# Kernel optimization log

Hardware: AMD Instinct MI355X
Metric: run time of the kernel (lower is better)

Reference implementation:

```python
import jax, jax.numpy as jnp
import numpy as np

# Module hyperparameters (match init_kwargs)
N_HEADS = 8
N_EMB = 64          # == window_size; unfolded window becomes the embed dim
WINDOW_SIZE = 64
STRIDE = 32
HEAD_DIM = N_EMB // N_HEADS


def _unfold_last(x):
    """torch.Tensor.unfold on last dim: [..., L] -> [..., NW, WINDOW_SIZE]."""
    L = x.shape[-1]
    starts = jnp.arange(0, L - WINDOW_SIZE + 1, STRIDE)          # [NW]
    idx = starts[:, None] + jnp.arange(WINDOW_SIZE)[None, :]     # [NW, WS]
    return x[..., idx]


def setup_inputs() -> dict:
    key = jax.random.key(0)
    ks = jax.random.split(key, 7)
    S, L = 512, 2048
    q = jax.random.normal(ks[0], (S, L), jnp.float32)
    k = jax.random.normal(ks[1], (S, L), jnp.float32)
    v = jax.random.normal(ks[2], (S, L), jnp.float32)
    scale = 1.0 / np.sqrt(N_EMB)
    in_proj_weight = jax.random.normal(ks[3], (3 * N_EMB, N_EMB), jnp.float32) * scale
    in_proj_bias = jax.random.normal(ks[4], (3 * N_EMB,), jnp.float32) * 0.02
    out_proj_weight = jax.random.normal(ks[5], (N_EMB, N_EMB), jnp.float32) * scale
    out_proj_bias = jax.random.normal(ks[6], (N_EMB,), jnp.float32) * 0.02
    return {"q": q, "k": k, "v": v,
            "in_proj_weight": in_proj_weight, "in_proj_bias": in_proj_bias,
            "out_proj_weight": out_proj_weight, "out_proj_bias": out_proj_bias}


def reference(q, k, v, in_proj_weight, in_proj_bias, out_proj_weight, out_proj_bias):
    # Unfold last dim into overlapping windows: [S, L] -> [S, NW, E]
    qu, ku, vu = _unfold_last(q), _unfold_last(k), _unfold_last(v)
    S, NW, E = qu.shape

    # nn.MultiheadAttention input projections (packed in_proj)
    Wq, Wk, Wv = jnp.split(in_proj_weight, 3, axis=0)
    bq, bk, bv = jnp.split(in_proj_bias, 3, axis=0)
    qp = qu @ Wq.T + bq   # [S, NW, E]
    kp = ku @ Wk.T + bk
    vp = vu @ Wv.T + bv

    # Split heads: [S, NW, E] -> [NW, H, S, HD]  (MHA: seq=S, batch=NW)
    def heads(x):
        return x.reshape(S, NW, N_HEADS, HEAD_DIM).transpose(1, 2, 0, 3)
    qh, kh, vh = heads(qp), heads(kp), heads(vp)

    scale = 1.0 / np.sqrt(HEAD_DIM)
    scores = jnp.einsum("nhsd,nhtd->nhst", qh, kh) * scale   # [NW, H, S, S]
    attn = jax.nn.softmax(scores, axis=-1)
    ctx = jnp.einsum("nhst,nhtd->nhsd", attn, vh)            # [NW, H, S, HD]

    # Merge heads back to [S, NW, E], then output projection
    ctx = ctx.transpose(2, 0, 1, 3).reshape(S, NW, E)
    x = ctx @ out_proj_weight.T + out_proj_bias              # [S, NW, E]

    # average_attn_weights=True (torch default): mean over heads -> [NW, S, S]
    attn_weights = attn.mean(axis=1)
    return x, attn_weights
```

## Files before the change

kernel.cpp:

```cpp
#include <hip/hip_runtime.h>

#define S_DIM 512
#define L_DIM 2048
#define NW 63
#define E_DIM 64

typedef __bf16 bf16_t;
typedef __bf16 bf16x8 __attribute__((ext_vector_type(8)));
typedef float f32x4 __attribute__((ext_vector_type(4)));
typedef _Float16 f16_t;
typedef _Float16 f16x2 __attribute__((ext_vector_type(2)));
typedef _Float16 f16x4 __attribute__((ext_vector_type(4)));

__device__ inline bf16x8 cvt8(const float* __restrict__ p) {
    float4 a = *(const float4*)p;
    float4 b = *(const float4*)(p + 4);
    bf16x8 r;
    r[0] = (bf16_t)a.x; r[1] = (bf16_t)a.y; r[2] = (bf16_t)a.z; r[3] = (bf16_t)a.w;
    r[4] = (bf16_t)b.x; r[5] = (bf16_t)b.y; r[6] = (bf16_t)b.z; r[7] = (bf16_t)b.w;
    return r;
}

__device__ inline f16x2 pkrtz(float a, float b) {
    return __builtin_bit_cast(f16x2, __builtin_amdgcn_cvt_pkrtz(a, b));
}

__global__ __launch_bounds__(512) void swa_proj(
    const float* __restrict__ q, const float* __restrict__ k,
    const float* __restrict__ v, const float* __restrict__ w,
    const float* __restrict__ bias,
    f16_t* __restrict__ qpg, f16_t* __restrict__ kpg, f16_t* __restrict__ vpg)
{
    __shared__ __align__(16) f16_t stq[128][72];
    __shared__ __align__(16) f16_t stk[128][72];
    __shared__ __align__(16) f16_t vt[64][136];

    int tid = threadIdx.x, lane = tid & 63, wave = tid >> 6;
    int bid = blockIdx.x;
    int n = bid >> 2, rg = bid & 3;
    int ml = lane & 15, quad = lane >> 4;
    int srow = wave * 16;
    int s0 = rg * 128 + srow;
    int arow = (s0 + ml) * L_DIM + 32 * n + quad * 8;
    const float cs = 0.35355339059327373f * 1.4426950408889634f;

    bf16x8 qa0 = cvt8(q + arow), qa1 = cvt8(q + arow + 32);
    bf16x8 ka0 = cvt8(k + arow), ka1 = cvt8(k + arow + 32);
    bf16x8 va0 = cvt8(v + arow), va1 = cvt8(v + arow + 32);

#pragma unroll
    for (int et = 0; et < 4; ++et) {
        bf16x8 wq0 = cvt8(w + (et * 16 + ml) * 64 + quad * 8);
        bf16x8 wq1 = cvt8(w + (et * 16 + ml) * 64 + 32 + quad * 8);
        bf16x8 wk0 = cvt8(w + (64 + et * 16 + ml) * 64 + quad * 8);
        bf16x8 wk1 = cvt8(w + (64 + et * 16 + ml) * 64 + 32 + quad * 8);
        bf16x8 wv0 = cvt8(w + (128 + et * 16 + ml) * 64 + quad * 8);
        bf16x8 wv1 = cvt8(w + (128 + et * 16 + ml) * 64 + 32 + quad * 8);

        float bq = bias[et * 16 + ml];
        float bk = bias[64 + et * 16 + ml];
        float bv = bias[128 + et * 16 + ml];
        f32x4 qacc = (f32x4){bq, bq, bq, bq};
        f32x4 kacc = (f32x4){bk, bk, bk, bk};
        f32x4 vacc = (f32x4){bv, bv, bv, bv};
        qacc = __builtin_amdgcn_mfma_f32_16x16x32_bf16(qa0, wq0, qacc, 0, 0, 0);
        qacc = __builtin_amdgcn_mfma_f32_16x16x32_bf16(qa1, wq1, qacc, 0, 0, 0);
        kacc = __builtin_amdgcn_mfma_f32_16x16x32_bf16(ka0, wk0, kacc, 0, 0, 0);
        kacc = __builtin_amdgcn_mfma_f32_16x16x32_bf16(ka1, wk1, kacc, 0, 0, 0);
        vacc = __builtin_amdgcn_mfma_f32_16x16x32_bf16(va0, wv0, vacc, 0, 0, 0);
        vacc = __builtin_amdgcn_mfma_f32_16x16x32_bf16(va1, wv1, vacc, 0, 0, 0);

#pragma unroll
        for (int rr = 0; rr < 4; ++rr) {
            int row = srow + quad * 4 + rr;
            stq[row][et * 16 + ml] = (f16_t)(qacc[rr] * cs);
            stk[row][et * 16 + ml] = (f16_t)kacc[rr];
            vt[et * 16 + ml][row]  = (f16_t)vacc[rr];
        }
    }
    __syncthreads();

    {
        const size_t qbase = ((size_t)n * S_DIM + rg * 128) * 64;
#pragma unroll
        for (int c = tid; c < 1024; c += 512) {
            int row = c >> 3, col = (c & 7) * 8;
            *(uint4*)(qpg + qbase + (size_t)row * 64 + col) = *(const uint4*)&stq[row][col];
        }
    }
    {
#pragma unroll
        for (int c = tid; c < 1024; c += 512) {
            int et = c >> 8, cc = c & 255, row = cc >> 1, hf = cc & 1;
            *(uint4*)(kpg + (((size_t)n * 4 + et) * S_DIM + rg * 128 + row) * 16 + hf * 8) =
                *(const uint4*)&stk[row][et * 16 + hf * 8];
        }
    }
    {
#pragma unroll
        for (int c = tid; c < 1024; c += 512) {
            int vr = c >> 4, sc = c & 15;
            *(uint4*)(vpg + (((size_t)n * 4 + (vr >> 4)) * 16 + (vr & 15)) * S_DIM +
                      rg * 128 + sc * 8) = *(const uint4*)&vt[vr][sc * 8];
        }
    }
}

__global__ __launch_bounds__(512, 2) void swa_attn(
    const f16_t* __restrict__ qpg, const f16_t* __restrict__ kpg,
    const f16_t* __restrict__ vpg, const float* __restrict__ wout,
    const float* __restrict__ bout, float* __restrict__ out)
{
    __shared__ __align__(16) f16_t kp_s[S_DIM][18];
    __shared__ __align__(16) f16_t vp_t[16][520];
    __shared__ __align__(16) f16_t qp_t[2][16][68];
    __shared__ __align__(16) f16_t zstub[8];
    __shared__ __align__(16) float wsum_s[2][2][16][4];
    __shared__ __align__(16) f16_t ctxslot[2][4][2][16][8];
    __shared__ float  ctx_s[32][68];
    __shared__ bf16_t wo_t[64][66];
    __shared__ float  bo_s[64];

    int tid = threadIdx.x, lane = tid & 63, wave = tid >> 6;
    int wg = wave >> 1, m = wave & 1;
    int bid = blockIdx.x;
    int n = bid >> 4, tile = bid & 15, srow0 = tile * 32;
    int ml = lane & 15, quad = lane >> 4;
    bool hi = lane >= 32;

    float* out_x  = out;
    float* out_aw = out + (size_t)S_DIM * NW * E_DIM;

#pragma unroll
    for (int i = 0; i < 8; ++i) {
        int idx = tid + i * 512;
        wo_t[idx & 63][idx >> 6] = (bf16_t)wout[idx];
    }
    if (tid < 64) bo_s[tid] = bout[tid];
    if (tid < 8)  zstub[tid] = (f16_t)0.f;
    {
        int row = tid >> 4, c = tid & 15;
        f16x4 qv = *(const f16x4*)(qpg + ((size_t)n * S_DIM + srow0 + row) * 64 + c * 4);
        *(f16x4*)&qp_t[row >> 4][row & 15][c * 4] = qv;
    }

    int idx0 = tid, idx1 = tid + 512;
    uint4 ldk0, ldk1, ldv0, ldv1;
    {
        const f16_t* kb = kpg + ((size_t)n * 4 + 0) * S_DIM * 16;
        ldk0 = *(const uint4*)(kb + (idx0 >> 1) * 16 + (idx0 & 1) * 8);
        ldk1 = *(const uint4*)(kb + (idx1 >> 1) * 16 + (idx1 & 1) * 8);
        const f16_t* vb = vpg + ((size_t)n * 4 + 0) * 16 * S_DIM;
        ldv0 = *(const uint4*)(vb + (idx0 >> 6) * S_DIM + (idx0 & 63) * 8);
        ldv1 = *(const uint4*)(vb + (idx1 >> 6) * S_DIM + (idx1 & 63) * 8);
    }

    f32x4 aacc[8];
#pragma unroll
    for (int t = 0; t < 8; ++t) aacc[t] = (f32x4){0.f, 0.f, 0.f, 0.f};

    for (int hp = 0; hp < 4; ++hp) {
        *(uint4*)&kp_s[idx0 >> 1][(idx0 & 1) * 8] = ldk0;
        *(uint4*)&kp_s[idx1 >> 1][(idx1 & 1) * 8] = ldk1;
        *(uint4*)&vp_t[idx0 >> 6][(idx0 & 63) * 8] = ldv0;
        *(uint4*)&vp_t[idx1 >> 6][(idx1 & 63) * 8] = ldv1;
        if (hp < 3) {
            const f16_t* kb = kpg + ((size_t)n * 4 + hp + 1) * S_DIM * 16;
            ldk0 = *(const uint4*)(kb + (idx0 >> 1) * 16 + (idx0 & 1) * 8);
            ldk1 = *(const uint4*)(kb + (idx1 >> 1) * 16 + (idx1 & 1) * 8);
            const f16_t* vb = vpg + ((size_t)n * 4 + hp + 1) * 16 * S_DIM;
            ldv0 = *(const uint4*)(vb + (idx0 >> 6) * S_DIM + (idx0 & 63) * 8);
            ldv1 = *(const uint4*)(vb + (idx1 >> 6) * S_DIM + (idx1 & 63) * 8);
        }
        __syncthreads();

        if (hp > 0) {
            int mm = tid >> 8, qq = (tid >> 4) & 15, hh = (tid >> 3) & 1, dd = tid & 7;
            ctx_s[mm * 16 + qq][(2 * (hp - 1) + hh) * 8 + dd] =
                (float)ctxslot[hh][0][mm][qq][dd] + (float)ctxslot[hh][1][mm][qq][dd] +
                (float)ctxslot[hh][2][mm][qq][dd] + (float)ctxslot[hh][3][mm][qq][dd];
        }

#pragma unroll
        for (int h01 = 0; h01 < 2; ++h01) {
            int h = hp * 2 + h01;

            const f16_t* qsrc = hi ? &zstub[0] : &qp_t[m][ml][h * 8 + quad * 4];
            f16x4 Qf = *(const f16x4*)qsrc;
            const f16_t* kbase = hi ? &zstub[0] : &kp_s[wg * 128 + ml][h01 * 8 + quad * 4];
            int kstep = hi ? 0 : 16 * 18;
            f32x4 S[8];
#pragma unroll
            for (int t = 0; t < 8; ++t) {
                f16x4 Kf = *(const f16x4*)(kbase + t * kstep);
                S[t] = __builtin_amdgcn_mfma_f32_16x16x16f16(Kf, Qf, (f32x4){0.f, 0.f, 0.f, 0.f}, 0, 0, 0);
            }

#pragma unroll
            for (int t = 0; t < 8; ++t) {
                S[t][0] = exp2f(S[t][0]);
                S[t][1] = exp2f(S[t][1]);
                S[t][2] = exp2f(S[t][2]);
                S[t][3] = exp2f(S[t][3]);
            }
            f32x4 sA = ((S[0] + S[1]) + (S[2] + S[3])) + ((S[4] + S[5]) + (S[6] + S[7]));
            float ls = (sA[0] + sA[1]) + (sA[2] + sA[3]);
            ls += __shfl_xor(ls, 16, 64);
            ls += __shfl_xor(ls, 32, 64);
            if (lane < 16) wsum_s[h & 1][m][lane][wg] = ls;

            const f16_t* vbase = &vp_t[h01 * 8 + (ml & 7)][wg * 128 + quad * 4];
            f32x4 cacc = (f32x4){0.f, 0.f, 0.f, 0.f};
#pragma unroll
            for (int t = 0; t < 8; ++t) {
                f16x4 Af = *(const f16x4*)(vbase + t * 16);
                f16x2 plo = pkrtz(S[t][0], S[t][1]);
                f16x2 phi = pkrtz(S[t][2], S[t][3]);
                f16x4 Pf = __builtin_shufflevector(plo, phi, 0, 1, 2, 3);
                cacc = __builtin_amdgcn_mfma_f32_16x16x16f16(Af, Pf, cacc, 0, 0, 0);
            }
            __syncthreads();

            f32x4 ws4 = *(const f32x4*)&wsum_s[h & 1][m][ml][0];
            float inv = 1.0f / ((ws4[0] + ws4[1]) + (ws4[2] + ws4[3]));

            float wgt = 0.125f * inv;
            f32x4 wv = (f32x4){wgt, wgt, wgt, wgt};
#pragma unroll
            for (int t = 0; t < 8; ++t)
                aacc[t] = __builtin_elementwise_fma(S[t], wv, aacc[t]);

            cacc = cacc * (f32x4){inv, inv, inv, inv};
            if (lane < 32) {
                f16x4 cw;
                cw[0] = (f16_t)cacc[0]; cw[1] = (f16_t)cacc[1];
                cw[2] = (f16_t)cacc[2]; cw[3] = (f16_t)cacc[3];
                *(f16x4*)&ctxslot[h01][wg][m][ml][quad * 4] = cw;
            }
        }
    }

    __syncthreads();
    {
        int mm = tid >> 8, qq = (tid >> 4) & 15, hh = (tid >> 3) & 1, dd = tid & 7;
        ctx_s[mm * 16 + qq][(6 + hh) * 8 + dd] =
            (float)ctxslot[hh][0][mm][qq][dd] + (float)ctxslot[hh][1][mm][qq][dd] +
            (float)ctxslot[hh][2][mm][qq][dd] + (float)ctxslot[hh][3][mm][qq][dd];
    }

    {
        int row = srow0 + m * 16 + ml;
        float* dst = out_aw + ((size_t)(n * S_DIM + row)) * S_DIM + wg * 128 + quad * 4;
#pragma unroll
        for (int t = 0; t < 8; ++t)
            *(f32x4*)&dst[t * 16] = aacc[t];
    }
    __syncthreads();

    int so = tid >> 4;
    int eb = tid & 15;
    float xacc[4];
#pragma unroll
    for (int kk = 0; kk < 4; ++kk) xacc[kk] = bo_s[eb + 16 * kk];
#pragma unroll
    for (int f = 0; f < 64; ++f) {
        float c = ctx_s[so][f];
#pragma unroll
        for (int kk = 0; kk < 4; ++kk)
            xacc[kk] = fmaf(c, (float)wo_t[f][eb + 16 * kk], xacc[kk]);
    }
    int sg = srow0 + so;
#pragma unroll
    for (int kk = 0; kk < 4; ++kk)
        out_x[((size_t)sg * NW + n) * E_DIM + eb + 16 * kk] = xacc[kk];
}

extern "C" void kernel_launch(void* const* d_in, const int* in_sizes, int n_in,
                              void* d_out, int out_size, void* d_ws, size_t ws_size,
                              hipStream_t stream) {
    const float* q  = (const float*)d_in[0];
    const float* k  = (const float*)d_in[1];
    const float* v  = (const float*)d_in[2];
    const float* w  = (const float*)d_in[3];
    const float* b  = (const float*)d_in[4];
    const float* wo = (const float*)d_in[5];
    const float* bo = (const float*)d_in[6];
    float* out = (float*)d_out;

    const size_t NP = (size_t)NW * S_DIM * 64;
    f16_t* qpg = (f16_t*)d_ws;
    f16_t* kpg = qpg + NP;
    f16_t* vpg = kpg + NP;

    hipLaunchKernelGGL(swa_proj, dim3(NW * 4), dim3(512), 0, stream,
                       q, k, v, w, b, qpg, kpg, vpg);
    hipLaunchKernelGGL(swa_attn, dim3(NW * 16), dim3(512), 0, stream,
                       qpg, kpg, vpg, wo, bo, out);
}
```

Baseline: 193.6 us.

## Use 16x16x32 f16 MFMA for PV and remap key rows to match

The P·V product now runs as four 16x16x32 MFMAs instead of eight 16x16x16 ones. To do that, the key rows feeding the QK MFMAs are permuted so each lane's score outputs line up with 8 contiguous V columns, and the attention-weight stores are reordered to match. Launch bounds also rise from 2 to 4 blocks per CU, which tightens the register budget and risks spills.

```diff
diff --git a/kernel.cpp b/kernel.cpp
--- a/kernel.cpp
+++ b/kernel.cpp
@@ -11,6 +11,7 @@
 typedef _Float16 f16_t;
 typedef _Float16 f16x2 __attribute__((ext_vector_type(2)));
 typedef _Float16 f16x4 __attribute__((ext_vector_type(4)));
+typedef _Float16 f16x8 __attribute__((ext_vector_type(8)));
 
 __device__ inline bf16x8 cvt8(const float* __restrict__ p) {
     float4 a = *(const float4*)p;
@@ -106,7 +107,7 @@
     }
 }
 
-__global__ __launch_bounds__(512, 2) void swa_attn(
+__global__ __launch_bounds__(512, 4) void swa_attn(
     const f16_t* __restrict__ qpg, const f16_t* __restrict__ kpg,
     const f16_t* __restrict__ vpg, const float* __restrict__ wout,
     const float* __restrict__ bout, float* __restrict__ out)
@@ -155,9 +156,14 @@
         ldv1 = *(const uint4*)(vb + (idx1 >> 6) * S_DIM + (idx1 & 63) * 8);
     }
 
-    f32x4 aacc[8];
-#pragma unroll
-    for (int t = 0; t < 8; ++t) aacc[t] = (f32x4){0.f, 0.f, 0.f, 0.f};
+    f32x4 aacc[4][2];
+#pragma unroll
+    for (int t = 0; t < 4; ++t) {
+        aacc[t][0] = (f32x4){0.f, 0.f, 0.f, 0.f};
+        aacc[t][1] = (f32x4){0.f, 0.f, 0.f, 0.f};
+    }
+
+    int krow = 8 * (ml >> 2) + (ml & 3);
 
     for (int hp = 0; hp < 4; ++hp) {
         *(uint4*)&kp_s[idx0 >> 1][(idx0 & 1) * 8] = ldk0;
@@ -187,37 +193,49 @@
 
             const f16_t* qsrc = hi ? &zstub[0] : &qp_t[m][ml][h * 8 + quad * 4];
             f16x4 Qf = *(const f16x4*)qsrc;
-            const f16_t* kbase = hi ? &zstub[0] : &kp_s[wg * 128 + ml][h01 * 8 + quad * 4];
-            int kstep = hi ? 0 : 16 * 18;
-            f32x4 S[8];
-#pragma unroll
-            for (int t = 0; t < 8; ++t) {
-                f16x4 Kf = *(const f16x4*)(kbase + t * kstep);
-                S[t] = __builtin_amdgcn_mfma_f32_16x16x16f16(Kf, Qf, (f32x4){0.f, 0.f, 0.f, 0.f}, 0, 0, 0);
+            const f16_t* kbase = hi ? &zstub[0]
+                                    : &kp_s[wg * 128 + krow][h01 * 8 + quad * 4];
+            int kwstep = hi ? 0 : 32 * 18;
+            int k4     = hi ? 0 : 4 * 18;
+
+            f32x4 SC[4][2];
+#pragma unroll
+            for (int t = 0; t < 4; ++t) {
+                f16x4 K1 = *(const f16x4*)(kbase + t * kwstep);
+                f16x4 K2 = *(const f16x4*)(kbase + t * kwstep + k4);
+                SC[t][0] = __builtin_amdgcn_mfma_f32_16x16x16f16(K1, Qf, (f32x4){0.f,0.f,0.f,0.f}, 0, 0, 0);
+                SC[t][1] = __builtin_amdgcn_mfma_f32_16x16x16f16(K2, Qf, (f32x4){0.f,0.f,0.f,0.f}, 0, 0, 0);
             }
 
 #pragma unroll
-            for (int t = 0; t < 8; ++t) {
-                S[t][0] = exp2f(S[t][0]);
-                S[t][1] = exp2f(S[t][1]);
-                S[t][2] = exp2f(S[t][2]);
-                S[t][3] = exp2f(S[t][3]);
-            }
-            f32x4 sA = ((S[0] + S[1]) + (S[2] + S[3])) + ((S[4] + S[5]) + (S[6] + S[7]));
+            for (int t = 0; t < 4; ++t)
+#pragma unroll
+                for (int c = 0; c < 2; ++c) {
+                    SC[t][c][0] = exp2f(SC[t][c][0]);
+                    SC[t][c][1] = exp2f(SC[t][c][1]);
+                    SC[t][c][2] = exp2f(SC[t][c][2]);
+                    SC[t][c][3] = exp2f(SC[t][c][3]);
+                }
+            f32x4 sA = ((SC[0][0] + SC[0][1]) + (SC[1][0] + SC[1][1])) +
+                       ((SC[2][0] + SC[2][1]) + (SC[3][0] + SC[3][1]));
             float ls = (sA[0] + sA[1]) + (sA[2] + sA[3]);
             ls += __shfl_xor(ls, 16, 64);
             ls += __shfl_xor(ls, 32, 64);
             if (lane < 16) wsum_s[h & 1][m][lane][wg] = ls;
 
-            const f16_t* vbase = &vp_t[h01 * 8 + (ml & 7)][wg * 128 + quad * 4];
+            const f16_t* vbase = &vp_t[h01 * 8 + (ml & 7)][wg * 128 + quad * 8];
             f32x4 cacc = (f32x4){0.f, 0.f, 0.f, 0.f};
 #pragma unroll
-            for (int t = 0; t < 8; ++t) {
-                f16x4 Af = *(const f16x4*)(vbase + t * 16);
-                f16x2 plo = pkrtz(S[t][0], S[t][1]);
-                f16x2 phi = pkrtz(S[t][2], S[t][3]);
-                f16x4 Pf = __builtin_shufflevector(plo, phi, 0, 1, 2, 3);
-                cacc = __builtin_amdgcn_mfma_f32_16x16x16f16(Af, Pf, cacc, 0, 0, 0);
+            for (int t = 0; t < 4; ++t) {
+                f16x8 Af = *(const f16x8*)(vbase + t * 32);
+                f16x2 p0 = pkrtz(SC[t][0][0], SC[t][0][1]);
+                f16x2 p1 = pkrtz(SC[t][0][2], SC[t][0][3]);
+                f16x2 p2 = pkrtz(SC[t][1][0], SC[t][1][1]);
+                f16x2 p3 = pkrtz(SC[t][1][2], SC[t][1][3]);
+                f16x8 Pf;
+                Pf[0] = p0[0]; Pf[1] = p0[1]; Pf[2] = p1[0]; Pf[3] = p1[1];
+                Pf[4] = p2[0]; Pf[5] = p2[1]; Pf[6] = p3[0]; Pf[7] = p3[1];
+                cacc = __builtin_amdgcn_mfma_f32_16x16x32_f16(Af, Pf, cacc, 0, 0, 0);
             }
             __syncthreads();
 
@@ -227,8 +245,10 @@
             float wgt = 0.125f * inv;
             f32x4 wv = (f32x4){wgt, wgt, wgt, wgt};
 #pragma unroll
-            for (int t = 0; t < 8; ++t)
-                aacc[t] = __builtin_elementwise_fma(S[t], wv, aacc[t]);
+            for (int t = 0; t < 4; ++t) {
+                aacc[t][0] = __builtin_elementwise_fma(SC[t][0], wv, aacc[t][0]);
+                aacc[t][1] = __builtin_elementwise_fma(SC[t][1], wv, aacc[t][1]);
+            }
 
             cacc = cacc * (f32x4){inv, inv, inv, inv};
             if (lane < 32) {
@@ -250,10 +270,12 @@
 
     {
         int row = srow0 + m * 16 + ml;
-        float* dst = out_aw + ((size_t)(n * S_DIM + row)) * S_DIM + wg * 128 + quad * 4;
-#pragma unroll
-        for (int t = 0; t < 8; ++t)
-            *(f32x4*)&dst[t * 16] = aacc[t];
+        float* dst = out_aw + ((size_t)(n * S_DIM + row)) * S_DIM + wg * 128 + quad * 8;
+#pragma unroll
+        for (int t = 0; t < 4; ++t) {
+            *(f32x4*)&dst[t * 32]     = aacc[t][0];
+            *(f32x4*)&dst[t * 32 + 4] = aacc[t][1];
+        }
     }
     __syncthreads();
 
```

After: 348.7 us. 1.8x slower.
